# Performance work log

Measured on AMD Instinct MI355X. Metric: run time of the kernel, lower is better.

The kernel has to match this reference:

```python
import jax, jax.numpy as jnp
import numpy as np

B, T, F = 8192, 200, 16
H = 32  # LSTM units
D = 60  # 6 * FREQUENCY


def setup_inputs() -> dict:
    key = jax.random.key(0)
    ks = jax.random.split(key, 5)
    s = 0.1
    return {
        "x": jax.random.normal(ks[0], (B, T, F), jnp.float32),
        "W": jax.random.normal(ks[1], (F, 4 * H), jnp.float32) * s,
        "U": jax.random.normal(ks[2], (H, 4 * H), jnp.float32) * s,
        "b": jnp.zeros((4 * H,), jnp.float32),
        "W1": jax.random.normal(ks[3], (H, D), jnp.float32) * s,
        "b1": jnp.zeros((D,), jnp.float32),
        "W2": jax.random.normal(ks[4], (H, D), jnp.float32) * s,
        "b2": jnp.zeros((D,), jnp.float32),
    }


def _lstm_last(x, W, U, b):
    # Precompute input-to-gate projections for all timesteps: [B, T, 4H]
    xg = jnp.einsum('btf,fg->btg', x, W) + b
    batch = x.shape[0]
    h0 = jnp.zeros((batch, H), x.dtype)
    c0 = jnp.zeros((batch, H), x.dtype)

    def step(carry, xg_t):
        h, c = carry
        g = xg_t + h @ U  # [B, 4H]
        i, f, cc, o = jnp.split(g, 4, axis=-1)  # Keras gate order: i, f, c, o
        i = jax.nn.sigmoid(i)
        f = jax.nn.sigmoid(f)
        o = jax.nn.sigmoid(o)
        c_new = f * c + i * jax.nn.relu(cc)  # activation=relu
        h_new = o * jax.nn.relu(c_new)
        return (h_new, c_new), None

    (h_T, _), _ = jax.lax.scan(step, (h0, c0), jnp.swapaxes(xg, 0, 1))
    return h_T  # return_sequences=False -> last hidden state [B, H]


def reference(x, W, U, b, W1, b1, W2, b2):
    h = _lstm_last(x, W, U, b)
    long_pred = h @ W1 + b1
    lat_pred = h @ W2 + b2
    return (long_pred, lat_pred)
```

## Files before the change

kernel.cpp:

```cpp
#include <hip/hip_runtime.h>

#define BATCH 8192
#define TSTEPS 200
#define FEAT 16
#define HID 32
#define GATES 128
#define DOUT 60
#define ROWS 16
#define HSTRIDE 40

typedef __fp16 half2v __attribute__((ext_vector_type(2)));
typedef __fp16 half4v __attribute__((ext_vector_type(4)));
typedef __fp16 half8v __attribute__((ext_vector_type(8)));
typedef float  float2v __attribute__((ext_vector_type(2)));
typedef float  float4v __attribute__((ext_vector_type(4)));

__device__ __forceinline__ half2v pkrtz(float a, float b) {
    return __builtin_amdgcn_cvt_pkrtz(a, b);
}

__device__ __forceinline__ half4v pack4(float4 v) {
    half2v lo = pkrtz(v.x, v.y);
    half2v hi = pkrtz(v.z, v.w);
    half4v r;
    r[0] = lo[0]; r[1] = lo[1]; r[2] = hi[0]; r[3] = hi[1];
    return r;
}

__device__ __forceinline__ int gcol(int tt, int m) {
    return 32 * (tt >> 1) + 8 * (m >> 2) + (m & 3) + 4 * (tt & 1);
}

union hUn { half8v v; half2v h2[4]; };

template <bool DO_XW, bool DO_LOAD, int LOFF>
__device__ __forceinline__ void lstm_step(
    float4& XN, const float* xp,
    const half8v (&bU)[8], const half4v (&bW)[8], const float4v (&bias)[8],
    float4v (&accx)[8], hUn& hB, float2v (&cst)[2][2])
{
    float4v acc[8];
    #pragma unroll
    for (int tt = 0; tt < 8; tt++)
        acc[tt] = __builtin_amdgcn_mfma_f32_16x16x32_f16(
            bU[tt], hB.v, accx[tt], 0, 0, 0);

    if (DO_XW) {
        half4v ax = pack4(XN);
        #pragma unroll
        for (int tt = 0; tt < 8; tt++)
            accx[tt] = __builtin_amdgcn_mfma_f32_16x16x16f16(
                bW[tt], ax, bias[tt], 0, 0, 0);
    }
    if (DO_LOAD)
        XN = *reinterpret_cast<const float4*>(xp + LOFF);

    float2v ei[2][2], ef[2][2], eo[2][2];
    #pragma unroll
    for (int hf = 0; hf < 2; hf++)
        #pragma unroll
        for (int p = 0; p < 2; p++) {
            ei[hf][p][0] = __builtin_amdgcn_exp2f(acc[0 + hf][2 * p]);
            ei[hf][p][1] = __builtin_amdgcn_exp2f(acc[0 + hf][2 * p + 1]);
            ef[hf][p][0] = __builtin_amdgcn_exp2f(acc[2 + hf][2 * p]);
            ef[hf][p][1] = __builtin_amdgcn_exp2f(acc[2 + hf][2 * p + 1]);
            eo[hf][p][0] = __builtin_amdgcn_exp2f(acc[6 + hf][2 * p]);
            eo[hf][p][1] = __builtin_amdgcn_exp2f(acc[6 + hf][2 * p + 1]);
        }

    const float2v one  = {1.0f, 1.0f};
    const float2v zero = {0.0f, 0.0f};
    #pragma unroll
    for (int hf = 0; hf < 2; hf++)
        #pragma unroll
        for (int p = 0; p < 2; p++) {
            float2v di  = one + ei[hf][p];
            float2v df  = one + ef[hf][p];
            float2v dov = one + eo[hf][p];
            float2v cc2 = {acc[4 + hf][2 * p], acc[4 + hf][2 * p + 1]};
            float2v rc  = __builtin_elementwise_max(cc2, zero);
            float2v num = __builtin_elementwise_fma(cst[hf][p], di, rc * df);
            float2v ee  = (di * df) * dov;
            float   Q   = __builtin_amdgcn_rcpf(ee[0] * ee[1]);
            float2v ie  = {Q * ee[1], Q * ee[0]};
            float2v c2  = num * (ie * dov);
            cst[hf][p]  = c2;
            float2v h2  = __builtin_elementwise_max(num, zero) * ie;
            hB.h2[2 * hf + p] = pkrtz(h2[0], h2[1]);
        }
}

__global__ __launch_bounds__(64, 1) void lstm_mfma(
    const float* __restrict__ x,
    const float* __restrict__ W,
    const float* __restrict__ U,
    const float* __restrict__ bg,
    const float* __restrict__ W1,
    const float* __restrict__ b1,
    const float* __restrict__ W2,
    const float* __restrict__ b2,
    float* __restrict__ out)
{
    const int lane = threadIdx.x;
    const int n16  = lane & 15;
    const int g    = lane >> 4;
    const int b0   = blockIdx.x * ROWS;

    __shared__ __align__(16) __fp16 hbuf[ROWS * HSTRIDE];

    half8v  bU[8];
    half4v  bW[8];
    float4v bias[8];
    #pragma unroll
    for (int tt = 0; tt < 8; tt++) {
        const float s = ((tt >> 1) == 2) ? 1.0f : -1.44269504088896340736f;
        const int colA = gcol(tt, n16);
        half8v u8;
        #pragma unroll
        for (int j = 0; j < 8; j++)
            u8[j] = (__fp16)(U[(8 * g + j) * GATES + colA] * s);
        bU[tt] = u8;
        half4v w4;
        #pragma unroll
        for (int j = 0; j < 4; j++)
            w4[j] = (__fp16)(W[(4 * g + j) * GATES + colA] * s);
        bW[tt] = w4;
        float4v bv;
        #pragma unroll
        for (int r = 0; r < 4; r++)
            bv[r] = bg[gcol(tt, 4 * g + r)] * s;
        bias[tt] = bv;
    }

    const float* xrow = x + (size_t)(b0 + n16) * TSTEPS * FEAT + 4 * g;

    float4 xf0 = *reinterpret_cast<const float4*>(xrow + FEAT);
    float4 xf1 = *reinterpret_cast<const float4*>(xrow + 2 * FEAT);

    float4v accx[8];
    {
        half4v a0 = pack4(*reinterpret_cast<const float4*>(xrow));
        #pragma unroll
        for (int tt = 0; tt < 8; tt++)
            accx[tt] = __builtin_amdgcn_mfma_f32_16x16x16f16(
                bW[tt], a0, bias[tt], 0, 0, 0);
    }

    hUn hB;
    hB.v = (half8v)(__fp16)0.f;
    float2v cst[2][2] = {{{0.f, 0.f}, {0.f, 0.f}}, {{0.f, 0.f}, {0.f, 0.f}}};

    const float* xp = xrow;
    for (int it = 0; it < (TSTEPS - 4) / 2; ++it) {
        lstm_step<true, true, 3 * FEAT>(xf0, xp, bU, bW, bias, accx, hB, cst);
        lstm_step<true, true, 4 * FEAT>(xf1, xp, bU, bW, bias, accx, hB, cst);
        xp += 2 * FEAT;
    }
    lstm_step<true, true, 3 * FEAT>(xf0, xp, bU, bW, bias, accx, hB, cst);
    lstm_step<true, false, 0>(xf1, xp, bU, bW, bias, accx, hB, cst);
    lstm_step<true, false, 0>(xf0, xp, bU, bW, bias, accx, hB, cst);
    lstm_step<false, false, 0>(xf1, xp, bU, bW, bias, accx, hB, cst);

    *reinterpret_cast<half8v*>(&hbuf[n16 * HSTRIDE + 8 * g]) = hB.v;
    __builtin_amdgcn_wave_barrier();

    for (int idx = lane; idx < ROWS * DOUT; idx += 64) {
        const int row = idx / DOUT;
        const int d   = idx - row * DOUT;
        float s1 = b1[d], s2 = b2[d];
        #pragma unroll 8
        for (int k = 0; k < HID; k++) {
            float hv = (float)hbuf[row * HSTRIDE + k];
            s1 = fmaf(hv, W1[k * DOUT + d], s1);
            s2 = fmaf(hv, W2[k * DOUT + d], s2);
        }
        out[(size_t)(b0 + row) * DOUT + d] = s1;
        out[(size_t)BATCH * DOUT + (size_t)(b0 + row) * DOUT + d] = s2;
    }
}

extern "C" void kernel_launch(void* const* d_in, const int* in_sizes, int n_in,
                              void* d_out, int out_size, void* d_ws, size_t ws_size,
                              hipStream_t stream) {
    const float* x  = (const float*)d_in[0];
    const float* W  = (const float*)d_in[1];
    const float* U  = (const float*)d_in[2];
    const float* bg = (const float*)d_in[3];
    const float* W1 = (const float*)d_in[4];
    const float* b1 = (const float*)d_in[5];
    const float* W2 = (const float*)d_in[6];
    const float* b2 = (const float*)d_in[7];
    float* out = (float*)d_out;

    dim3 grid(BATCH / ROWS);
    dim3 block(64);
    lstm_mfma<<<grid, block, 0, stream>>>(x, W, U, bg, W1, b1, W2, b2, out);
}
```

Measured before the change: 232.6 us.

## Split LSTM gate columns across two waves with LDS double-buffered hidden state

Each block now runs two wavefronts instead of one. Each wave owns half of the hidden units' gate columns, so it issues 4 MFMAs per step instead of 8 and does half the activation math. The hidden state is exchanged every timestep through a double-buffered LDS array with a __syncthreads barrier. This cuts the per-wave serial dependency chain, at the cost of an LDS round trip and a block barrier on every recurrent step.

New measurement: 255.0 us. +9.6%, slower.

```diff
diff --git a/kernel.cpp b/kernel.cpp
--- a/kernel.cpp
+++ b/kernel.cpp
@@ -27,70 +27,62 @@
     return r;
 }
 
-__device__ __forceinline__ int gcol(int tt, int m) {
-    return 32 * (tt >> 1) + 8 * (m >> 2) + (m & 3) + 4 * (tt & 1);
-}
-
-union hUn { half8v v; half2v h2[4]; };
-
 template <bool DO_XW, bool DO_LOAD, int LOFF>
 __device__ __forceinline__ void lstm_step(
     float4& XN, const float* xp,
-    const half8v (&bU)[8], const half4v (&bW)[8], const float4v (&bias)[8],
-    float4v (&accx)[8], hUn& hB, float2v (&cst)[2][2])
+    const half8v (&aU)[4], const half4v (&aW)[4], const float4v (&bias)[4],
+    float4v (&accx)[4], float2v (&cst)[2],
+    const __fp16* hr, __fp16* hw, int hroff, int hwoff)
 {
-    float4v acc[8];
+    half8v hB = *reinterpret_cast<const half8v*>(&hr[hroff]);
+
+    float4v acc[4];
     #pragma unroll
-    for (int tt = 0; tt < 8; tt++)
+    for (int tt = 0; tt < 4; tt++)
         acc[tt] = __builtin_amdgcn_mfma_f32_16x16x32_f16(
-            bU[tt], hB.v, accx[tt], 0, 0, 0);
+            aU[tt], hB, accx[tt], 0, 0, 0);
 
     if (DO_XW) {
         half4v ax = pack4(XN);
         #pragma unroll
-        for (int tt = 0; tt < 8; tt++)
+        for (int tt = 0; tt < 4; tt++)
             accx[tt] = __builtin_amdgcn_mfma_f32_16x16x16f16(
-                bW[tt], ax, bias[tt], 0, 0, 0);
+                aW[tt], ax, bias[tt], 0, 0, 0);
     }
     if (DO_LOAD)
         XN = *reinterpret_cast<const float4*>(xp + LOFF);
 
-    float2v ei[2][2], ef[2][2], eo[2][2];
-    #pragma unroll
-    for (int hf = 0; hf < 2; hf++)
-        #pragma unroll
-        for (int p = 0; p < 2; p++) {
-            ei[hf][p][0] = __builtin_amdgcn_exp2f(acc[0 + hf][2 * p]);
-            ei[hf][p][1] = __builtin_amdgcn_exp2f(acc[0 + hf][2 * p + 1]);
-            ef[hf][p][0] = __builtin_amdgcn_exp2f(acc[2 + hf][2 * p]);
-            ef[hf][p][1] = __builtin_amdgcn_exp2f(acc[2 + hf][2 * p + 1]);
-            eo[hf][p][0] = __builtin_amdgcn_exp2f(acc[6 + hf][2 * p]);
-            eo[hf][p][1] = __builtin_amdgcn_exp2f(acc[6 + hf][2 * p + 1]);
-        }
-
     const float2v one  = {1.0f, 1.0f};
     const float2v zero = {0.0f, 0.0f};
+    union { half4v v; half2v h2[2]; } hv;
     #pragma unroll
-    for (int hf = 0; hf < 2; hf++)
-        #pragma unroll
-        for (int p = 0; p < 2; p++) {
-            float2v di  = one + ei[hf][p];
-            float2v df  = one + ef[hf][p];
-            float2v dov = one + eo[hf][p];
-            float2v cc2 = {acc[4 + hf][2 * p], acc[4 + hf][2 * p + 1]};
-            float2v rc  = __builtin_elementwise_max(cc2, zero);
-            float2v num = __builtin_elementwise_fma(cst[hf][p], di, rc * df);
-            float2v ee  = (di * df) * dov;
-            float   Q   = __builtin_amdgcn_rcpf(ee[0] * ee[1]);
-            float2v ie  = {Q * ee[1], Q * ee[0]};
-            float2v c2  = num * (ie * dov);
-            cst[hf][p]  = c2;
-            float2v h2  = __builtin_elementwise_max(num, zero) * ie;
-            hB.h2[2 * hf + p] = pkrtz(h2[0], h2[1]);
-        }
-}
-
-__global__ __launch_bounds__(64, 1) void lstm_mfma(
+    for (int p = 0; p < 2; p++) {
+        float2v ei, ef, eo;
+        ei[0] = __builtin_amdgcn_exp2f(acc[0][2 * p]);
+        ei[1] = __builtin_amdgcn_exp2f(acc[0][2 * p + 1]);
+        ef[0] = __builtin_amdgcn_exp2f(acc[1][2 * p]);
+        ef[1] = __builtin_amdgcn_exp2f(acc[1][2 * p + 1]);
+        eo[0] = __builtin_amdgcn_exp2f(acc[3][2 * p]);
+        eo[1] = __builtin_amdgcn_exp2f(acc[3][2 * p + 1]);
+        float2v di  = one + ei;
+        float2v df  = one + ef;
+        float2v dov = one + eo;
+        float2v cc2 = {acc[2][2 * p], acc[2][2 * p + 1]};
+        float2v rc  = __builtin_elementwise_max(cc2, zero);
+        float2v num = __builtin_elementwise_fma(cst[p], di, rc * df);
+        float2v ee  = (di * df) * dov;
+        float   Q   = __builtin_amdgcn_rcpf(ee[0] * ee[1]);
+        float2v ie  = {Q * ee[1], Q * ee[0]};
+        float2v c2  = num * (ie * dov);
+        cst[p] = c2;
+        float2v h2  = __builtin_elementwise_max(num, zero) * ie;
+        hv.h2[p] = pkrtz(h2[0], h2[1]);
+    }
+    *reinterpret_cast<half4v*>(&hw[hwoff]) = hv.v;
+    __syncthreads();
+}
+
+__global__ __launch_bounds__(128, 1) void lstm_mfma(
     const float* __restrict__ x,
     const float* __restrict__ W,
     const float* __restrict__ U,
@@ -101,76 +93,86 @@
     const float* __restrict__ b2,
     float* __restrict__ out)
 {
-    const int lane = threadIdx.x;
+    const int tid  = threadIdx.x;
+    const int lane = tid & 63;
+    const int w    = tid >> 6;
     const int n16  = lane & 15;
     const int g    = lane >> 4;
     const int b0   = blockIdx.x * ROWS;
 
-    __shared__ __align__(16) __fp16 hbuf[ROWS * HSTRIDE];
-
-    half8v  bU[8];
-    half4v  bW[8];
-    float4v bias[8];
+    __shared__ __align__(16) __fp16 hbuf[2][ROWS * HSTRIDE];
+
+    half8v  aU[4];
+    half4v  aW[4];
+    float4v bias[4];
     #pragma unroll
-    for (int tt = 0; tt < 8; tt++) {
-        const float s = ((tt >> 1) == 2) ? 1.0f : -1.44269504088896340736f;
-        const int colA = gcol(tt, n16);
+    for (int tt = 0; tt < 4; tt++) {
+        const float s = (tt == 2) ? 1.0f : -1.44269504088896340736f;
+        const int colA = 32 * tt + 16 * w + n16;
         half8v u8;
         #pragma unroll
         for (int j = 0; j < 8; j++)
             u8[j] = (__fp16)(U[(8 * g + j) * GATES + colA] * s);
-        bU[tt] = u8;
+        aU[tt] = u8;
         half4v w4;
         #pragma unroll
         for (int j = 0; j < 4; j++)
             w4[j] = (__fp16)(W[(4 * g + j) * GATES + colA] * s);
-        bW[tt] = w4;
+        aW[tt] = w4;
         float4v bv;
         #pragma unroll
         for (int r = 0; r < 4; r++)
-            bv[r] = bg[gcol(tt, 4 * g + r)] * s;
+            bv[r] = bg[32 * tt + 16 * w + 4 * g + r] * s;
         bias[tt] = bv;
     }
+
+    for (int i = tid; i < ROWS * HSTRIDE; i += 128) hbuf[0][i] = (__fp16)0.f;
 
     const float* xrow = x + (size_t)(b0 + n16) * TSTEPS * FEAT + 4 * g;
 
     float4 xf0 = *reinterpret_cast<const float4*>(xrow + FEAT);
     float4 xf1 = *reinterpret_cast<const float4*>(xrow + 2 * FEAT);
 
-    float4v accx[8];
+    float4v accx[4];
     {
         half4v a0 = pack4(*reinterpret_cast<const float4*>(xrow));
         #pragma unroll
-        for (int tt = 0; tt < 8; tt++)
+        for (int tt = 0; tt < 4; tt++)
             accx[tt] = __builtin_amdgcn_mfma_f32_16x16x16f16(
-                bW[tt], a0, bias[tt], 0, 0, 0);
-    }
-
-    hUn hB;
-    hB.v = (half8v)(__fp16)0.f;
-    float2v cst[2][2] = {{{0.f, 0.f}, {0.f, 0.f}}, {{0.f, 0.f}, {0.f, 0.f}}};
+                aW[tt], a0, bias[tt], 0, 0, 0);
+    }
+
+    float2v cst[2] = {{0.f, 0.f}, {0.f, 0.f}};
+    const int hroff = n16 * HSTRIDE + 8 * g;
+    const int hwoff = n16 * HSTRIDE + 16 * w + 4 * g;
+
+    __syncthreads();
 
     const float* xp = xrow;
     for (int it = 0; it < (TSTEPS - 4) / 2; ++it) {
-        lstm_step<true, true, 3 * FEAT>(xf0, xp, bU, bW, bias, accx, hB, cst);
-        lstm_step<true, true, 4 * FEAT>(xf1, xp, bU, bW, bias, accx, hB, cst);
+        lstm_step<true, true, 3 * FEAT>(xf0, xp, aU, aW, bias, accx, cst,
+                                        hbuf[0], hbuf[1], hroff, hwoff);
+        lstm_step<true, true, 4 * FEAT>(xf1, xp, aU, aW, bias, accx, cst,
+                                        hbuf[1], hbuf[0], hroff, hwoff);
         xp += 2 * FEAT;
     }
-    lstm_step<true, true, 3 * FEAT>(xf0, xp, bU, bW, bias, accx, hB, cst);
-    lstm_step<true, false, 0>(xf1, xp, bU, bW, bias, accx, hB, cst);
-    lstm_step<true, false, 0>(xf0, xp, bU, bW, bias, accx, hB, cst);
-    lstm_step<false, false, 0>(xf1, xp, bU, bW, bias, accx, hB, cst);
-
-    *reinterpret_cast<half8v*>(&hbuf[n16 * HSTRIDE + 8 * g]) = hB.v;
-    __builtin_amdgcn_wave_barrier();
-
-    for (int idx = lane; idx < ROWS * DOUT; idx += 64) {
+    lstm_step<true, true, 3 * FEAT>(xf0, xp, aU, aW, bias, accx, cst,
+                                    hbuf[0], hbuf[1], hroff, hwoff);
+    lstm_step<true, false, 0>(xf1, xp, aU, aW, bias, accx, cst,
+                              hbuf[1], hbuf[0], hroff, hwoff);
+    lstm_step<true, false, 0>(xf0, xp, aU, aW, bias, accx, cst,
+                              hbuf[0], hbuf[1], hroff, hwoff);
+    lstm_step<false, false, 0>(xf1, xp, aU, aW, bias, accx, cst,
+                               hbuf[1], hbuf[0], hroff, hwoff);
+
+    const __fp16* hf = &hbuf[0][0];
+    for (int idx = tid; idx < ROWS * DOUT; idx += 128) {
         const int row = idx / DOUT;
         const int d   = idx - row * DOUT;
         float s1 = b1[d], s2 = b2[d];
         #pragma unroll 8
         for (int k = 0; k < HID; k++) {
-            float hv = (float)hbuf[row * HSTRIDE + k];
+            float hv = (float)hf[row * HSTRIDE + k];
             s1 = fmaf(hv, W1[k * DOUT + d], s1);
             s2 = fmaf(hv, W2[k * DOUT + d], s2);
         }
@@ -193,6 +195,6 @@
     float* out = (float*)d_out;
 
     dim3 grid(BATCH / ROWS);
-    dim3 block(64);
+    dim3 block(128);
     lstm_mfma<<<grid, block, 0, stream>>>(x, W, U, bg, W1, b1, W2, b2, out);
 }
```
